# Performance work log

Measured on AMD Instinct MI355X. Metric: run time of the kernel, lower is better.

## Reference

```python
import jax, jax.numpy as jnp
import numpy as np

N_NODES = 100_000
N_EDGES = 1_600_000
N_GRAPHS = 64
N_OPS = 120
OP_EMB = 32
NODE_FEAT = 140
CFG_FEAT = 18
LIN_OUT = 128
H = 64
EPS = 1e-12  # F.normalize eps


def _glorot(k, shape):
    s = (6.0 / (shape[0] + shape[1])) ** 0.5
    return jax.random.uniform(k, shape, jnp.float32, -s, s)


def setup_inputs() -> dict:
    key = jax.random.key(0)
    ks = iter(jax.random.split(key, 40))
    inp = {
        "node_feat": jax.random.normal(next(ks), (N_NODES, NODE_FEAT), jnp.float32),
        "node_config_feat": jax.random.normal(next(ks), (N_NODES, CFG_FEAT), jnp.float32),
        "node_opcode": jax.random.randint(next(ks), (N_NODES,), 0, N_OPS, jnp.int32),
        "edge_index": jax.random.randint(next(ks), (2, N_EDGES), 0, N_NODES, jnp.int32),
        # contiguous graph assignment -> every one of the 64 graphs is non-empty
        "batch": ((jnp.arange(N_NODES) * N_GRAPHS) // N_NODES).astype(jnp.int32),
        "op_emb": jax.random.normal(next(ks), (N_OPS, OP_EMB), jnp.float32),
        "lin_w": _glorot(next(ks), (NODE_FEAT + OP_EMB + CFG_FEAT, LIN_OUT)),
        "lin_b": jnp.zeros((LIN_OUT,), jnp.float32),
        "post_w": _glorot(next(ks), (H, 1)),
        "post_b": jnp.zeros((1,), jnp.float32),
    }
    in_dims = [LIN_OUT, H, H]
    for l, d in enumerate(in_dims):
        inp[f"proj_w{l}"] = _glorot(next(ks), (d, d))
        inp[f"proj_b{l}"] = jnp.zeros((d,), jnp.float32)
        inp[f"wl{l}"] = _glorot(next(ks), (d, H))
        inp[f"bl{l}"] = jnp.zeros((H,), jnp.float32)
        inp[f"wr{l}"] = _glorot(next(ks), (d, H))
    return inp


def _sage_conv(x, src, dst, pw, pb, wl, bl, wr):
    # PyG SAGEConv(normalize=True, project=True): messages use projected x,
    # root term uses the un-projected x; mean aggregation over in-edges.
    xp = jax.nn.relu(x @ pw + pb)                                  # (N, d)
    msg = jax.ops.segment_sum(xp[src], dst, num_segments=N_NODES)  # (N, d)
    deg = jax.ops.segment_sum(jnp.ones((src.shape[0],), x.dtype), dst,
                              num_segments=N_NODES)
    mean = msg / jnp.maximum(deg, 1.0)[:, None]
    out = mean @ wl + bl + x @ wr                                   # (N, H)
    n = jnp.linalg.norm(out, axis=-1, keepdims=True)
    return out / jnp.maximum(n, EPS)


def reference(node_feat, node_config_feat, node_opcode, edge_index, batch,
              op_emb, lin_w, lin_b, post_w, post_b,
              proj_w0, proj_b0, wl0, bl0, wr0,
              proj_w1, proj_b1, wl1, bl1, wr1,
              proj_w2, proj_b2, wl2, bl2, wr2):
    x = jnp.concatenate([node_feat, op_emb[node_opcode], node_config_feat], axis=-1)
    x = jax.nn.relu(x @ lin_w + lin_b)  # (N, 128)
    src, dst = edge_index[0], edge_index[1]
    layers = [(proj_w0, proj_b0, wl0, bl0, wr0),
              (proj_w1, proj_b1, wl1, bl1, wr1),
              (proj_w2, proj_b2, wl2, bl2, wr2)]
    for pw, pb, wl, bl, wr in layers:
        x = _sage_conv(x, src, dst, pw, pb, wl, bl, wr)
    # global max pool + global mean pool per graph
    x_max = jax.ops.segment_max(x, batch, num_segments=N_GRAPHS)
    cnt = jax.ops.segment_sum(jnp.ones((x.shape[0],), x.dtype), batch,
                              num_segments=N_GRAPHS)
    x_mean = jax.ops.segment_sum(x, batch, num_segments=N_GRAPHS) / cnt[:, None]
    x_graph = x_max + x_mean
    x_graph = x_graph / jnp.linalg.norm(x_graph, axis=-1, keepdims=True)
    return x_graph @ post_w + post_b  # (B, 1)
```

## Files before the change

### kernel.cpp

```cpp
#include <hip/hip_runtime.h>
#include <hip/hip_bf16.h>
#include <math.h>

#define N_NODES   100000
#define N_EDGES   1600000
#define N_GRAPHS  64
#define NF_D      140
#define OP_EMB_D  32
#define CFG_D     18
#define K_EMB     192
#define NB_SCAN   391

typedef __attribute__((ext_vector_type(8))) short short8;
typedef __attribute__((ext_vector_type(4))) float f32x4;

__device__ __forceinline__ unsigned fenc(float f) {
    unsigned u = __float_as_uint(f);
    return (u & 0x80000000u) ? ~u : (u | 0x80000000u);
}
__device__ __forceinline__ float fdec(unsigned u) {
    unsigned v = (u & 0x80000000u) ? (u & 0x7FFFFFFFu) : ~u;
    return __uint_as_float(v);
}
__device__ __forceinline__ unsigned short f2bf(float f) {
    unsigned u = __float_as_uint(f);
    return (unsigned short)((u + 0x7FFFu + ((u >> 16) & 1u)) >> 16);
}
__device__ __forceinline__ float bf2f(unsigned short h) {
    return __uint_as_float((unsigned)h << 16);
}
__device__ __forceinline__ short8 ld_frag(const unsigned short* p) {
    union { uint4 u; short8 s; } c;
    c.u = *(const uint4*)p;
    return c.s;
}


__global__ void hist_kernel(const int* __restrict__ dst, int* __restrict__ cnt) {
    int e = blockIdx.x * blockDim.x + threadIdx.x;
    if (e < N_EDGES) atomicAdd(&cnt[dst[e]], 1);
}

__global__ __launch_bounds__(256) void blocksum_kernel(const int* __restrict__ cnt,
                                                       int* __restrict__ bsum) {
    const int tid = threadIdx.x, lane = tid & 63, wave = tid >> 6;
    int i = blockIdx.x * 256 + tid;
    int v = (i < N_NODES) ? cnt[i] : 0;
    #pragma unroll
    for (int off = 32; off > 0; off >>= 1) v += __shfl_xor(v, off, 64);
    __shared__ int wsum[4];
    if (lane == 0) wsum[wave] = v;
    __syncthreads();
    if (tid == 0) bsum[blockIdx.x] = wsum[0] + wsum[1] + wsum[2] + wsum[3];
}

__global__ __launch_bounds__(512) void scanbsum_kernel(int* __restrict__ bsum) {
    __shared__ int s[512];
    const int t = threadIdx.x;
    int v0 = (t < NB_SCAN) ? bsum[t] : 0;
    s[t] = v0;
    __syncthreads();
    for (int off = 1; off < 512; off <<= 1) {
        int add = (t >= off) ? s[t - off] : 0;
        __syncthreads();
        s[t] += add;
        __syncthreads();
    }
    if (t < NB_SCAN) bsum[t] = s[t] - v0;
}

__global__ __launch_bounds__(256) void offsets_kernel(int* __restrict__ cnt,
                                                      const int* __restrict__ bsum,
                                                      int* __restrict__ row_start) {
    const int t = threadIdx.x;
    const int i = blockIdx.x * 256 + t;
    int v0 = (i < N_NODES) ? cnt[i] : 0;
    __shared__ int s[256];
    s[t] = v0;
    __syncthreads();
    for (int off = 1; off < 256; off <<= 1) {
        int add = (t >= off) ? s[t - off] : 0;
        __syncthreads();
        s[t] += add;
        __syncthreads();
    }
    const int excl = s[t] - v0 + bsum[blockIdx.x];
    if (i < N_NODES) {
        row_start[i] = excl;
        cnt[i] = excl;
    }
    if (i == N_NODES - 1) row_start[N_NODES] = excl + v0;
}

__global__ void fill_kernel(const int* __restrict__ src, const int* __restrict__ dst,
                            int* __restrict__ cursor, int* __restrict__ nbr) {
    const int range = blockIdx.x & 7;
    const int lo = range * (N_NODES / 8);
    const int hi = lo + (N_NODES / 8);
    const int groups = gridDim.x >> 3;
    const int sub = blockIdx.x >> 3;
    for (int e = sub * blockDim.x + threadIdx.x; e < N_EDGES;
         e += groups * blockDim.x) {
        const int d = dst[e];
        if (d >= lo && d < hi) {
            const int slot = atomicAdd(&cursor[d], 1);
            nbr[slot] = src[e];
        }
    }
}


__global__ __launch_bounds__(256) void concat_kernel(
    const float* __restrict__ node_feat, const float* __restrict__ cfg,
    const int* __restrict__ opcode, const float* __restrict__ op_emb,
    unsigned short* __restrict__ x0)
{
    const long long total = (long long)N_NODES * 96;
    for (long long idx = (long long)blockIdx.x * blockDim.x + threadIdx.x;
         idx < total; idx += (long long)gridDim.x * blockDim.x) {
        const int n  = (int)(idx / 96);
        const int c  = 2 * (int)(idx % 96);
        float2 v;
        if (c < NF_D) {
            v = *(const float2*)(node_feat + (long long)n * NF_D + c);
        } else if (c < NF_D + OP_EMB_D) {
            const int op = opcode[n];
            v = *(const float2*)(op_emb + op * OP_EMB_D + (c - NF_D));
        } else if (c < 190) {
            v = *(const float2*)(cfg + (long long)n * CFG_D + (c - NF_D - OP_EMB_D));
        } else {
            v.x = 0.f; v.y = 0.f;
        }
        const unsigned pk = ((unsigned)f2bf(v.y) << 16) | (unsigned)f2bf(v.x);
        *(unsigned*)(x0 + (long long)n * K_EMB + c) = pk;
    }
}

struct WDesc { const float* src; unsigned short* dst; int K, Ksrc, M, off; };
struct WPack { WDesc d[10]; int total; };

__global__ __launch_bounds__(256) void pack_w_kernel(WPack p) {
    const int idx = blockIdx.x * blockDim.x + threadIdx.x;
    if (idx >= p.total) return;
    #pragma unroll
    for (int i = 0; i < 10; ++i) {
        const WDesc d = p.d[i];
        if (idx >= d.off && idx < d.off + d.K * d.M) {
            const int r    = idx - d.off;
            const int kc   = r / (d.M * 32);
            const int rem  = r % (d.M * 32);
            const int mt   = rem / 512;
            const int rem2 = rem % 512;
            const int lane = rem2 >> 3;
            const int j    = rem2 & 7;
            const int k = kc * 32 + (lane >> 4) * 8 + j;
            const int m = mt * 16 + (lane & 15);
            const float v = (k < d.Ksrc) ? d.src[(long long)k * d.M + m] : 0.f;
            d.dst[r] = f2bf(v);
            return;
        }
    }
}

template <int M, int K, bool BIAS, bool RELU, bool OBF16>
__global__ __launch_bounds__(256) void mfma_gemm(
    const unsigned short* __restrict__ x,
    const unsigned short* __restrict__ wpk, const float* __restrict__ b,
    void* __restrict__ outv, int N)
{
    constexpr int MT = M / 16;
    constexpr int KC = K / 32;
    const int tid = threadIdx.x, wave = tid >> 6, lane = tid & 63;
    const int wid = blockIdx.x * 4 + wave;
    if (wid >= (N >> 5)) return;
    const int nb   = wid << 5;
    const int l15  = lane & 15;
    const int quad = lane >> 4;

    f32x4 acc[2][MT];
    #pragma unroll
    for (int mt = 0; mt < MT; ++mt) {
        #pragma unroll
        for (int r = 0; r < 4; ++r) {
            const float bv = BIAS ? b[mt * 16 + quad * 4 + r] : 0.f;
            acc[0][mt][r] = bv;
            acc[1][mt][r] = bv;
        }
    }
    #pragma unroll
    for (int kc = 0; kc < KC; ++kc) {
        const short8 b0 = ld_frag(x + (long long)(nb + l15)      * K + kc * 32 + quad * 8);
        const short8 b1 = ld_frag(x + (long long)(nb + 16 + l15) * K + kc * 32 + quad * 8);
        #pragma unroll
        for (int mt = 0; mt < MT; ++mt) {
            const short8 a = ld_frag(wpk + ((long long)(kc * MT + mt) * 64 + lane) * 8);
            acc[0][mt] = __builtin_amdgcn_mfma_f32_16x16x32_bf16(a, b0, acc[0][mt], 0, 0, 0);
            acc[1][mt] = __builtin_amdgcn_mfma_f32_16x16x32_bf16(a, b1, acc[1][mt], 0, 0, 0);
        }
    }
    #pragma unroll
    for (int s = 0; s < 2; ++s) {
        const long long row = nb + s * 16 + l15;
        if (OBF16) {
            unsigned short* orow = (unsigned short*)outv + row * M;
            #pragma unroll
            for (int mt = 0; mt < MT; ++mt) {
                float f0 = acc[s][mt][0], f1 = acc[s][mt][1];
                float f2 = acc[s][mt][2], f3 = acc[s][mt][3];
                if (RELU) {
                    f0 = fmaxf(f0, 0.f); f1 = fmaxf(f1, 0.f);
                    f2 = fmaxf(f2, 0.f); f3 = fmaxf(f3, 0.f);
                }
                uint2 pk;
                pk.x = ((unsigned)f2bf(f1) << 16) | (unsigned)f2bf(f0);
                pk.y = ((unsigned)f2bf(f3) << 16) | (unsigned)f2bf(f2);
                *(uint2*)(orow + mt * 16 + quad * 4) = pk;
            }
        } else {
            float* orow = (float*)outv + row * M;
            #pragma unroll
            for (int mt = 0; mt < MT; ++mt) {
                f32x4 v = acc[s][mt];
                if (RELU) {
                    v[0] = fmaxf(v[0], 0.f); v[1] = fmaxf(v[1], 0.f);
                    v[2] = fmaxf(v[2], 0.f); v[3] = fmaxf(v[3], 0.f);
                }
                *(f32x4*)(orow + mt * 16 + quad * 4) = v;
            }
        }
    }
}

template <bool OBF16>
__global__ __launch_bounds__(256, 8) void combine_kernel(
    const int* __restrict__ row_start, const int* __restrict__ nbr,
    const unsigned short* __restrict__ yp, const float* __restrict__ r,
    void* __restrict__ out)
{
    const int tid = threadIdx.x, wave = tid >> 6, lane = tid & 63;
    for (int n = blockIdx.x * 4 + wave; n < N_NODES; n += gridDim.x * 4) {
        const int rs = row_start[n], re = row_start[n + 1];
        float macc[8];
        #pragma unroll
        for (int q = 0; q < 8; ++q) macc[q] = 0.f;
        for (int eb = rs; eb < re; eb += 64) {
            const int cnt = min(64, re - eb);
            const int my = (eb + lane < re) ? nbr[eb + lane] : 0;
            for (int j2 = 0; j2 < cnt; j2 += 8) {
                #pragma unroll
                for (int q = 0; q < 8; ++q) {
                    const int jj = j2 + q;
                    const int s = __shfl(my, (jj < cnt) ? jj : 0, 64);
                    const float v = bf2f(yp[(long long)s * 64 + lane]);
                    if (jj < cnt) macc[q] += v;
                }
            }
        }
        const float m = ((macc[0] + macc[1]) + (macc[2] + macc[3]))
                      + ((macc[4] + macc[5]) + (macc[6] + macc[7]));
        float acc = r[(long long)n * 64 + lane] + m / fmaxf((float)(re - rs), 1.0f);
        float sq = acc * acc;
        #pragma unroll
        for (int off = 32; off > 0; off >>= 1) sq += __shfl_xor(sq, off, 64);
        const float res = acc / fmaxf(sqrtf(sq), 1e-12f);
        if (OBF16)
            ((unsigned short*)out)[(long long)n * 64 + lane] = f2bf(res);
        else
            ((float*)out)[(long long)n * 64 + lane] = res;
    }
}


__global__ __launch_bounds__(256) void pool_kernel(
    const float* __restrict__ x, const int* __restrict__ batch,
    float* __restrict__ gsum, unsigned* __restrict__ gmax, float* __restrict__ gcnt)
{
    __shared__ float    lsum[2][64];
    __shared__ unsigned lmax[2][64];
    __shared__ int      lcnt[2];
    const int tid = threadIdx.x, wave = tid >> 6, lane = tid & 63;
    if (tid < 128) { lsum[tid >> 6][tid & 63] = 0.f; lmax[tid >> 6][tid & 63] = 0u; }
    if (tid < 2) lcnt[tid] = 0;
    __syncthreads();
    const int base = blockIdx.x * 256;
    const int g0 = batch[base];
    float a0 = 0.f, a1 = 0.f, x0 = -INFINITY, x1 = -INFINITY;
    int c0 = 0, c1 = 0;
    for (int nn = 0; nn < 64; ++nn) {
        const int n = base + wave * 64 + nn;
        if (n >= N_NODES) break;
        const float v = x[(long long)n * 64 + lane];
        const int slot = batch[n] - g0;
        if (slot == 0)      { a0 += v; x0 = fmaxf(x0, v); c0++; }
        else if (slot == 1) { a1 += v; x1 = fmaxf(x1, v); c1++; }
        else {
            const int g = g0 + slot;
            atomicAdd(&gsum[g * 64 + lane], v);
            atomicMax(&gmax[g * 64 + lane], fenc(v));
            if (lane == 0) atomicAdd(&gcnt[g], 1.f);
        }
    }
    if (c0) { atomicAdd(&lsum[0][lane], a0); atomicMax(&lmax[0][lane], fenc(x0));
              if (lane == 0) atomicAdd(&lcnt[0], c0); }
    if (c1) { atomicAdd(&lsum[1][lane], a1); atomicMax(&lmax[1][lane], fenc(x1));
              if (lane == 0) atomicAdd(&lcnt[1], c1); }
    __syncthreads();
    if (tid < 128) {
        const int slot = tid >> 6, k = tid & 63;
        if (lcnt[slot] > 0) {
            const int g = g0 + slot;
            atomicAdd(&gsum[g * 64 + k], lsum[slot][k]);
            atomicMax(&gmax[g * 64 + k], lmax[slot][k]);
            if (k == 0) atomicAdd(&gcnt[g], (float)lcnt[slot]);
        }
    }
}

__global__ void finalize_kernel(const float* __restrict__ gsum, const unsigned* __restrict__ gmax,
                                const float* __restrict__ gcnt, const float* __restrict__ post_w,
                                const float* __restrict__ post_b, float* __restrict__ out)
{
    const int g = blockIdx.x;
    const int k = threadIdx.x;
    const float cnt = gcnt[g];
    const float v = fdec(gmax[g * 64 + k]) + gsum[g * 64 + k] / cnt;
    const float w = post_w[k];
    float sq = v * v, dw = v * w;
    #pragma unroll
    for (int off = 32; off > 0; off >>= 1) {
        sq += __shfl_xor(sq, off, 64);
        dw += __shfl_xor(dw, off, 64);
    }
    if (k == 0) out[g] = dw / sqrtf(sq) + post_b[0];
}

extern "C" void kernel_launch(void* const* d_in, const int* in_sizes, int n_in,
                              void* d_out, int out_size, void* d_ws, size_t ws_size,
                              hipStream_t stream)
{
    const float* node_feat = (const float*)d_in[0];
    const float* cfg       = (const float*)d_in[1];
    const int*   opcode    = (const int*)  d_in[2];
    const int*   edge      = (const int*)  d_in[3];
    const int*   batch     = (const int*)  d_in[4];
    const float* op_emb    = (const float*)d_in[5];
    const float* lin_w     = (const float*)d_in[6];
    const float* lin_b     = (const float*)d_in[7];
    const float* post_w    = (const float*)d_in[8];
    const float* post_b    = (const float*)d_in[9];
    const float* pw[3] = {(const float*)d_in[10], (const float*)d_in[15], (const float*)d_in[20]};
    const float* pb[3] = {(const float*)d_in[11], (const float*)d_in[16], (const float*)d_in[21]};
    const float* wl[3] = {(const float*)d_in[12], (const float*)d_in[17], (const float*)d_in[22]};
    const float* bl[3] = {(const float*)d_in[13], (const float*)d_in[18], (const float*)d_in[23]};
    const float* wr[3] = {(const float*)d_in[14], (const float*)d_in[19], (const float*)d_in[24]};
    const int* srcp = edge;
    const int* dstp = edge + N_EDGES;

    float* ws   = (float*)d_ws;
    int*   nbr       = (int*)(ws + 32000000);
    int*   row_start = (int*)(ws + 33600000);
    int*   cnt       = (int*)(ws + 33700064);
    int*   bsum      = (int*)(ws + 33800064);
    float* gsum      = ws + 33825152;
    float* gcnt      = ws + 33829248;
    unsigned* gmax   = (unsigned*)(ws + 33829312);
    unsigned short* wpk_base = (unsigned short*)(ws + 34000000);

    const int OFF_EMB = 0;
    const int OFF_PW0 = 24576;
    const int OFF_WL0 = 24576 + 16384;
    const int OFF_WR0 = OFF_WL0 + 8192;
    const int OFF_PW1 = OFF_WR0 + 8192;
    const int OFF_WL1 = OFF_PW1 + 4096;
    const int OFF_WR1 = OFF_WL1 + 4096;
    const int OFF_PW2 = OFF_WR1 + 4096;
    const int OFF_WL2 = OFF_PW2 + 4096;
    const int OFF_WR2 = OFF_WL2 + 4096;
    const int W_TOTAL = OFF_WR2 + 4096;

    unsigned short* A_bf    = (unsigned short*)ws;
    unsigned short* C2_bf   = (unsigned short*)ws;
    float*          C3      = ws;
    unsigned short* C1_bf   = (unsigned short*)(ws + 6400000);
    unsigned short* X0_bf   = (unsigned short*)(ws + 12800000);
    unsigned short* xp128_bf= (unsigned short*)(ws + 12800000);
    unsigned short* xp64_bf = (unsigned short*)(ws + 12800000);
    float*          r       = ws + 19200000;
    unsigned short* yp      = (unsigned short*)(ws + 25600000);

    hipMemsetAsync(cnt, 0, (size_t)N_NODES * 4, stream);
    hipMemsetAsync(gsum, 0, (size_t)(4096 + 64 + 4096) * 4, stream);

    WPack wp;
    wp.d[0] = { lin_w, wpk_base + OFF_EMB, K_EMB, 190, 128, OFF_EMB };
    wp.d[1] = { pw[0], wpk_base + OFF_PW0, 128, 128, 128, OFF_PW0 };
    wp.d[2] = { wl[0], wpk_base + OFF_WL0, 128, 128,  64, OFF_WL0 };
    wp.d[3] = { wr[0], wpk_base + OFF_WR0, 128, 128,  64, OFF_WR0 };
    wp.d[4] = { pw[1], wpk_base + OFF_PW1,  64,  64,  64, OFF_PW1 };
    wp.d[5] = { wl[1], wpk_base + OFF_WL1,  64,  64,  64, OFF_WL1 };
    wp.d[6] = { wr[1], wpk_base + OFF_WR1,  64,  64,  64, OFF_WR1 };
    wp.d[7] = { pw[2], wpk_base + OFF_PW2,  64,  64,  64, OFF_PW2 };
    wp.d[8] = { wl[2], wpk_base + OFF_WL2,  64,  64,  64, OFF_WL2 };
    wp.d[9] = { wr[2], wpk_base + OFF_WR2,  64,  64,  64, OFF_WR2 };
    wp.total = W_TOTAL;
    pack_w_kernel<<<(W_TOTAL + 255) / 256, 256, 0, stream>>>(wp);

    hist_kernel<<<(N_EDGES + 255) / 256, 256, 0, stream>>>(dstp, cnt);
    blocksum_kernel<<<NB_SCAN, 256, 0, stream>>>(cnt, bsum);
    scanbsum_kernel<<<1, 512, 0, stream>>>(bsum);
    offsets_kernel<<<NB_SCAN, 256, 0, stream>>>(cnt, bsum, row_start);
    fill_kernel<<<8 * 104, 256, 0, stream>>>(srcp, dstp, cnt, nbr);

    concat_kernel<<<4096, 256, 0, stream>>>(node_feat, cfg, opcode, op_emb, X0_bf);

    const int GW = (N_NODES / 32 + 3) / 4;

    mfma_gemm<128, 192, true, true, true><<<GW, 256, 0, stream>>>(
        X0_bf, wpk_base + OFF_EMB, lin_b, A_bf, N_NODES);

    mfma_gemm<128, 128, true,  true,  true ><<<GW, 256, 0, stream>>>(
        A_bf, wpk_base + OFF_PW0, pb[0], xp128_bf, N_NODES);
    mfma_gemm< 64, 128, false, false, true ><<<GW, 256, 0, stream>>>(
        xp128_bf, wpk_base + OFF_WL0, nullptr, yp, N_NODES);
    mfma_gemm< 64, 128, true,  false, false><<<GW, 256, 0, stream>>>(
        A_bf, wpk_base + OFF_WR0, bl[0], r, N_NODES);
    combine_kernel<true><<<2048, 256, 0, stream>>>(row_start, nbr, yp, r, C1_bf);

    mfma_gemm< 64, 64, true,  true,  true ><<<GW, 256, 0, stream>>>(
        C1_bf, wpk_base + OFF_PW1, pb[1], xp64_bf, N_NODES);
    mfma_gemm< 64, 64, false, false, true ><<<GW, 256, 0, stream>>>(
        xp64_bf, wpk_base + OFF_WL1, nullptr, yp, N_NODES);
    mfma_gemm< 64, 64, true,  false, false><<<GW, 256, 0, stream>>>(
        C1_bf, wpk_base + OFF_WR1, bl[1], r, N_NODES);
    combine_kernel<true><<<2048, 256, 0, stream>>>(row_start, nbr, yp, r, C2_bf);

    mfma_gemm< 64, 64, true,  true,  true ><<<GW, 256, 0, stream>>>(
        C2_bf, wpk_base + OFF_PW2, pb[2], xp64_bf, N_NODES);
    mfma_gemm< 64, 64, false, false, true ><<<GW, 256, 0, stream>>>(
        xp64_bf, wpk_base + OFF_WL2, nullptr, yp, N_NODES);
    mfma_gemm< 64, 64, true,  false, false><<<GW, 256, 0, stream>>>(
        C2_bf, wpk_base + OFF_WR2, bl[2], r, N_NODES);
    combine_kernel<false><<<2048, 256, 0, stream>>>(row_start, nbr, yp, r, C3);

    pool_kernel<<<NB_SCAN, 256, 0, stream>>>(C3, batch, gsum, gmax, gcnt);
    finalize_kernel<<<N_GRAPHS, 64, 0, stream>>>(gsum, gmax, gcnt, post_w, post_b,
                                                 (float*)d_out);
}
```

Measured before the change: 659.8 us.

## Partition edges into destination bins before CSR fill to avoid rescanning edges

The degree histogram is merged with a one-pass partition kernel. Each block stages packed (dst, src) pairs in per-bin shared-memory buffers and flushes them to eight global destination-range buckets. The fill kernel then reads only its own bucket, so the old pattern of every range group scanning all 1.6M edges goes away. In exchange there is extra global traffic for the 8-byte packed pairs, shared-memory staging with block barriers, and a bucket buffer that aliases a workspace region later reused by activations.

```diff
diff --git a/kernel.cpp b/kernel.cpp
--- a/kernel.cpp
+++ b/kernel.cpp
@@ -10,6 +10,10 @@
 #define CFG_D     18
 #define K_EMB     192
 #define NB_SCAN   391
+#define NBINS     8
+#define BIN_W     12500
+#define BIN_CAP   512
+#define BKT_CAP   1600000LL
 
 typedef __attribute__((ext_vector_type(8))) short short8;
 typedef __attribute__((ext_vector_type(4))) float f32x4;
@@ -36,9 +40,55 @@
 }
 
 
-__global__ void hist_kernel(const int* __restrict__ dst, int* __restrict__ cnt) {
-    int e = blockIdx.x * blockDim.x + threadIdx.x;
-    if (e < N_EDGES) atomicAdd(&cnt[dst[e]], 1);
+__global__ __launch_bounds__(256) void partition_kernel(
+    const int* __restrict__ src, const int* __restrict__ dst,
+    int* __restrict__ cnt, unsigned long long* __restrict__ bkt,
+    int* __restrict__ bcur)
+{
+    __shared__ unsigned long long buf[NBINS][BIN_CAP];
+    __shared__ int bcnt[NBINS];
+    __shared__ int bbase[NBINS];
+    const int tid = threadIdx.x;
+    if (tid < NBINS) bcnt[tid] = 0;
+    __syncthreads();
+    const long long stride = (long long)gridDim.x * 256;
+    for (long long e0 = (long long)blockIdx.x * 256; e0 < N_EDGES; e0 += stride) {
+        const long long e = e0 + tid;
+        if (e < N_EDGES) {
+            const int d = dst[e];
+            const int s = src[e];
+            atomicAdd(&cnt[d], 1);
+            const int b = d / BIN_W;
+            const int slot = atomicAdd(&bcnt[b], 1);
+            buf[b][slot] = ((unsigned long long)(unsigned)d << 32) | (unsigned)s;
+        }
+        __syncthreads();
+        #pragma unroll
+        for (int b = 0; b < NBINS; ++b) {
+            const int c = bcnt[b];
+            if (c >= 256) {
+                if (tid == 0) bbase[b] = atomicAdd(&bcur[b], c);
+                __syncthreads();
+                const int base = bbase[b];
+                for (int i = tid; i < c; i += 256)
+                    bkt[(long long)b * BKT_CAP + base + i] = buf[b][i];
+                if (tid == 0) bcnt[b] = 0;
+            }
+        }
+        __syncthreads();
+    }
+    #pragma unroll
+    for (int b = 0; b < NBINS; ++b) {
+        const int c = bcnt[b];
+        if (c > 0) {
+            if (tid == 0) bbase[b] = atomicAdd(&bcur[b], c);
+            __syncthreads();
+            const int base = bbase[b];
+            for (int i = tid; i < c; i += 256)
+                bkt[(long long)b * BKT_CAP + base + i] = buf[b][i];
+        }
+        __syncthreads();
+    }
 }
 
 __global__ __launch_bounds__(256) void blocksum_kernel(const int* __restrict__ cnt,
@@ -92,20 +142,20 @@
     if (i == N_NODES - 1) row_start[N_NODES] = excl + v0;
 }
 
-__global__ void fill_kernel(const int* __restrict__ src, const int* __restrict__ dst,
-                            int* __restrict__ cursor, int* __restrict__ nbr) {
-    const int range = blockIdx.x & 7;
-    const int lo = range * (N_NODES / 8);
-    const int hi = lo + (N_NODES / 8);
+__global__ void fill2_kernel(const unsigned long long* __restrict__ bkt,
+                             const int* __restrict__ bcur,
+                             int* __restrict__ cursor, int* __restrict__ nbr)
+{
+    const int b = blockIdx.x & 7;
+    const int n = bcur[b];
     const int groups = gridDim.x >> 3;
     const int sub = blockIdx.x >> 3;
-    for (int e = sub * blockDim.x + threadIdx.x; e < N_EDGES;
-         e += groups * blockDim.x) {
-        const int d = dst[e];
-        if (d >= lo && d < hi) {
-            const int slot = atomicAdd(&cursor[d], 1);
-            nbr[slot] = src[e];
-        }
+    for (int i = sub * 256 + threadIdx.x; i < n; i += groups * 256) {
+        const unsigned long long pk = bkt[(long long)b * BKT_CAP + i];
+        const int d = (int)(pk >> 32);
+        const int s = (int)(pk & 0xffffffffu);
+        const int slot = atomicAdd(&cursor[d], 1);
+        nbr[slot] = s;
     }
 }
 
@@ -361,6 +411,7 @@
     int*   row_start = (int*)(ws + 33600000);
     int*   cnt       = (int*)(ws + 33700064);
     int*   bsum      = (int*)(ws + 33800064);
+    int*   bcur      = (int*)(ws + 33810000);
     float* gsum      = ws + 33825152;
     float* gcnt      = ws + 33829248;
     unsigned* gmax   = (unsigned*)(ws + 33829312);
@@ -378,6 +429,7 @@
     const int OFF_WR2 = OFF_WL2 + 4096;
     const int W_TOTAL = OFF_WR2 + 4096;
 
+    unsigned long long* bkt = (unsigned long long*)ws;
     unsigned short* A_bf    = (unsigned short*)ws;
     unsigned short* C2_bf   = (unsigned short*)ws;
     float*          C3      = ws;
@@ -389,6 +441,7 @@
     unsigned short* yp      = (unsigned short*)(ws + 25600000);
 
     hipMemsetAsync(cnt, 0, (size_t)N_NODES * 4, stream);
+    hipMemsetAsync(bcur, 0, 8 * 4, stream);
     hipMemsetAsync(gsum, 0, (size_t)(4096 + 64 + 4096) * 4, stream);
 
     WPack wp;
@@ -405,11 +458,11 @@
     wp.total = W_TOTAL;
     pack_w_kernel<<<(W_TOTAL + 255) / 256, 256, 0, stream>>>(wp);
 
-    hist_kernel<<<(N_EDGES + 255) / 256, 256, 0, stream>>>(dstp, cnt);
+    partition_kernel<<<1024, 256, 0, stream>>>(srcp, dstp, cnt, bkt, bcur);
     blocksum_kernel<<<NB_SCAN, 256, 0, stream>>>(cnt, bsum);
     scanbsum_kernel<<<1, 512, 0, stream>>>(bsum);
     offsets_kernel<<<NB_SCAN, 256, 0, stream>>>(cnt, bsum, row_start);
-    fill_kernel<<<8 * 104, 256, 0, stream>>>(srcp, dstp, cnt, nbr);
+    fill2_kernel<<<8 * 256, 256, 0, stream>>>(bkt, bcur, cnt, nbr);
 
     concat_kernel<<<4096, 256, 0, stream>>>(node_feat, cfg, opcode, op_emb, X0_bf);
 
```

Result: slower. 745.8 us (+13.0%).
